# Kernel tuning notes

Measured on AMD Instinct MI355X. Metric: run time of the kernel, lower is better.

## Reference

```python
import jax, jax.numpy as jnp
import numpy as np

D_MODEL = 1024
NUM_HEADS = 16
D_K = D_MODEL // NUM_HEADS
R = 8
ALPHA = 16
SCALING = ALPHA / R


def _lora_linear(x, W, b, A, Bm):
    # base: x @ W.T + b ; lora: (x @ A.T) @ Bm.T * scaling
    base = jnp.einsum('btd,od->bto', x, W) + b
    lora = jnp.einsum('btr,or->bto', jnp.einsum('btd,rd->btr', x, A), Bm) * SCALING
    return base + lora


def setup_inputs() -> dict:
    key = jax.random.key(0)
    ks = jax.random.split(key, 20)
    B, T = 2, 2048
    inp = {
        'q': jax.random.normal(ks[0], (B, T, D_MODEL), jnp.float32),
        'k': jax.random.normal(ks[1], (B, T, D_MODEL), jnp.float32),
        'v': jax.random.normal(ks[2], (B, T, D_MODEL), jnp.float32),
        'mask': jnp.ones((1, 1, T, T), jnp.int32),
    }
    i = 3
    for name in ('q', 'k', 'v'):
        inp[f'W{name}'] = jax.random.normal(ks[i], (D_MODEL, D_MODEL), jnp.float32) * 0.02; i += 1
        inp[f'b{name}'] = jnp.zeros((D_MODEL,), jnp.float32)
        inp[f'A{name}'] = jax.random.normal(ks[i], (R, D_MODEL), jnp.float32) * 0.01; i += 1
        inp[f'B{name}'] = jax.random.normal(ks[i], (D_MODEL, R), jnp.float32) * 0.01; i += 1
    inp['Wo'] = jax.random.normal(ks[i], (D_MODEL, D_MODEL), jnp.float32) * 0.02
    inp['bo'] = jnp.zeros((D_MODEL,), jnp.float32)
    return inp


def reference(q, k, v, mask, Wq, bq, Aq, Bq, Wk, bk, Ak, Bk, Wv, bv, Av, Bv, Wo, bo):
    B, Tq, _ = q.shape
    Tk = k.shape[1]
    Q = _lora_linear(q, Wq, bq, Aq, Bq).reshape(B, Tq, NUM_HEADS, D_K).transpose(0, 2, 1, 3)
    K = _lora_linear(k, Wk, bk, Ak, Bk).reshape(B, Tk, NUM_HEADS, D_K).transpose(0, 2, 1, 3)
    V = _lora_linear(v, Wv, bv, Av, Bv).reshape(B, Tk, NUM_HEADS, D_K).transpose(0, 2, 1, 3)
    scores = jnp.einsum('bhqd,bhkd->bhqk', Q, K) / jnp.sqrt(jnp.float32(D_K))
    scores = jnp.where(mask == 0, jnp.float32(-1e9), scores)
    attn = jax.nn.softmax(scores, axis=-1)
    out = jnp.einsum('bhqk,bhkd->bhqd', attn, V)
    out = out.transpose(0, 2, 1, 3).reshape(B, Tq, D_MODEL)
    return jnp.einsum('btd,od->bto', out, Wo) + bo
```

## Files before the change

### kernel.cpp

```cpp
#include <hip/hip_runtime.h>
#include <stdint.h>

typedef unsigned short u16;
typedef __attribute__((ext_vector_type(4))) float f32x4;
typedef __attribute__((ext_vector_type(4))) uint32_t u32x4;
typedef __attribute__((ext_vector_type(8))) __bf16 bf16x8;

#if __has_builtin(__builtin_amdgcn_exp2f)
#define EXP2(x) __builtin_amdgcn_exp2f(x)
#else
#define EXP2(x) exp2f(x)
#endif

static __device__ __forceinline__ u16 f2bf(float f) {
    union { float f; uint32_t i; } v; v.f = f;
    return (u16)((v.i + 0x7FFFu + ((v.i >> 16) & 1u)) >> 16);
}
static __device__ __forceinline__ uint32_t cvtpk(float lo, float hi) {
    uint32_t r;
    asm("v_cvt_pk_bf16_f32 %0, %1, %2" : "=v"(r) : "v"(lo), "v"(hi));
    return r;
}

static __device__ __forceinline__ void gl2lds16(const u16* g, u16* lds) {
    __builtin_amdgcn_global_load_lds(
        (const __attribute__((address_space(1))) void*)g,
        (__attribute__((address_space(3))) void*)lds, 16, 0, 0);
}

struct PrepArgs {
    const float* csrc[7]; u16* cdst[7];
    const float* A[3]; u16* apk[3];
    const int* mask; int* flags;
};

__global__ __launch_bounds__(256)
void prep_kernel(PrepArgs a) {
    const int bid = blockIdx.x;
    const int tid = threadIdx.x;

    if (bid < 1024) {
        int arr, boff;
        if (bid < 768) { arr = bid >> 8; boff = bid & 255; }
        else { int b2 = bid - 768; arr = 3 + (b2 >> 6); boff = b2 & 63; }
        const float* s = a.csrc[arr] + (size_t)boff * 16384;
        u16* d = a.cdst[arr] + (size_t)boff * 16384;
#pragma unroll
        for (int i = 0; i < 8; ++i) {
            int c = tid + i * 256;
            float4 f0 = *(const float4*)(s + c * 8);
            float4 f1 = *(const float4*)(s + c * 8 + 4);
            u16 o[8];
            o[0] = f2bf(f0.x); o[1] = f2bf(f0.y); o[2] = f2bf(f0.z); o[3] = f2bf(f0.w);
            o[4] = f2bf(f1.x); o[5] = f2bf(f1.y); o[6] = f2bf(f1.z); o[7] = f2bf(f1.w);
            *(uint4*)(d + c * 8) = *(const uint4*)o;
        }
    } else if (bid < 1536) {
        const int b3 = bid - 1024;
        const int qb = b3 & 15, kt = b3 >> 4;
        int ok = 1;
#pragma unroll
        for (int i = 0; i < 8; ++i) {
            int c = tid + i * 256;
            int row = c >> 4, cg = c & 15;
            int4 m4 = *(const int4*)&a.mask[(size_t)(qb * 128 + row) * 2048 + kt * 64 + cg * 4];
            ok &= (m4.x != 0) & (m4.y != 0) & (m4.z != 0) & (m4.w != 0);
        }
        int wall = __all(ok) ? 1 : 0;
        __shared__ int red[4];
        if ((tid & 63) == 0) red[tid >> 6] = wall;
        __syncthreads();
        if (tid == 0) a.flags[qb * 32 + kt] = red[0] & red[1] & red[2] & red[3];
    } else {
        const int z = bid - 1536;
        const float* Az = a.A[z];
        u16* dp = a.apk[z];
#pragma unroll
        for (int i = 0; i < 8; ++i) {
            int pos = tid + i * 256;
            int lane2 = pos & 63;
            int l15_ = lane2 & 15, l4_ = lane2 >> 4;
            int kbkk = pos >> 6;
            int kcol = (kbkk >> 1) * 64 + (kbkk & 1) * 32 + l4_ * 8;
            u16 ob[8] = {0, 0, 0, 0, 0, 0, 0, 0};
            if (l15_ < 8) {
                float4 f0 = *(const float4*)&Az[(size_t)l15_ * 1024 + kcol];
                float4 f1 = *(const float4*)&Az[(size_t)l15_ * 1024 + kcol + 4];
                ob[0] = f2bf(f0.x); ob[1] = f2bf(f0.y); ob[2] = f2bf(f0.z); ob[3] = f2bf(f0.w);
                ob[4] = f2bf(f1.x); ob[5] = f2bf(f1.y); ob[6] = f2bf(f1.z); ob[7] = f2bf(f1.w);
            }
            *(uint4*)&dp[(size_t)pos * 8] = *(const uint4*)ob;
        }
    }
}

struct GemmPtrs { const u16* X; const u16* W; const float* bias; const u16* Ap; const float* Bm; void* out; int transT; float oscale; };
struct GemmArgs { GemmPtrs p[3]; };

#define LST 136
#define LTT 72

template <int WMT, int WNT, int LORA>
__global__ __launch_bounds__(256, 2)
void gemm_kernel(GemmArgs args) {
    constexpr int BM = WMT * 32, BN = WNT * 32;
    constexpr int MBLK = 4096 / BM;
    constexpr int IPA = BM / 32;
    constexpr int IPB = BN / 32;
    __shared__ alignas(16) u16 smem[2][(BM + BN) * 64];

    const GemmPtrs gp = args.p[blockIdx.z];
    const int tid = threadIdx.x;
    const int lane = tid & 63, wave = tid >> 6;
    const int wm = wave >> 1, wn = wave & 1;
    const int l15 = lane & 15, l4 = lane >> 4;
    const int id = blockIdx.x;
    const int m0 = (id % MBLK) * BM, n0 = (id / MBLK) * BN;

    const int srow = lane >> 3;
    const int scol = ((lane & 7) ^ srow) * 8;
    const u16* gA[IPA];
    const u16* gB[IPB];
#pragma unroll
    for (int i = 0; i < IPA; ++i) {
        int q = wave * IPA + i;
        gA[i] = gp.X + (size_t)(m0 + q * 8 + srow) * 1024 + scol;
    }
#pragma unroll
    for (int i = 0; i < IPB; ++i) {
        int q = wave * IPB + i;
        gB[i] = gp.W + (size_t)(n0 + q * 8 + srow) * 1024 + scol;
    }

    const f32x4 fz = {0.f, 0.f, 0.f, 0.f};
    f32x4 acc[WMT][WNT];
#pragma unroll
    for (int i = 0; i < WMT; ++i)
#pragma unroll
        for (int j = 0; j < WNT; ++j) acc[i][j] = fz;
    f32x4 acc_xa[WMT];
    bf16x8 abf[2], abf_n[2];
    if constexpr (LORA) {
#pragma unroll
        for (int i = 0; i < WMT; ++i) acc_xa[i] = fz;
        abf[0] = *(const bf16x8*)&gp.Ap[(size_t)(0 * 64 + lane) * 8];
        abf[1] = *(const bf16x8*)&gp.Ap[(size_t)(1 * 64 + lane) * 8];
    }

#pragma unroll
    for (int i = 0; i < IPA; ++i)
        gl2lds16(gA[i], &smem[0][(wave * IPA + i) * 512]);
#pragma unroll
    for (int i = 0; i < IPB; ++i)
        gl2lds16(gB[i], &smem[0][BM * 64 + (wave * IPB + i) * 512]);
    __syncthreads();

    const int sw = l15 & 7;
    for (int kb = 0; kb < 16; ++kb) {
        const u16* As = &smem[kb & 1][0];
        const u16* Bs = &smem[kb & 1][BM * 64];

        if (kb < 15) {
            if constexpr (LORA) {
                abf_n[0] = *(const bf16x8*)&gp.Ap[(size_t)(((kb + 1) * 2 + 0) * 64 + lane) * 8];
                abf_n[1] = *(const bf16x8*)&gp.Ap[(size_t)(((kb + 1) * 2 + 1) * 64 + lane) * 8];
            }
            u16* An = &smem[(kb + 1) & 1][0];
            u16* Bn = &smem[(kb + 1) & 1][BM * 64];
#pragma unroll
            for (int i = 0; i < IPA; ++i)
                gl2lds16(gA[i] + (kb + 1) * 64, &An[(wave * IPA + i) * 512]);
#pragma unroll
            for (int i = 0; i < IPB; ++i)
                gl2lds16(gB[i] + (kb + 1) * 64, &Bn[(wave * IPB + i) * 512]);
        }

#pragma unroll
        for (int kk2 = 0; kk2 < 2; ++kk2) {
            bf16x8 af[WMT], bfr[WNT];
#pragma unroll
            for (int mt = 0; mt < WMT; ++mt) {
                int x = wm * (WMT * 16) + mt * 16 + l15;
                af[mt] = *(const bf16x8*)&As[x * 64 + (((kk2 * 4 + l4) ^ sw) * 8)];
            }
#pragma unroll
            for (int nt = 0; nt < WNT; ++nt) {
                int y = wn * (WNT * 16) + nt * 16 + l15;
                bfr[nt] = *(const bf16x8*)&Bs[y * 64 + (((kk2 * 4 + l4) ^ sw) * 8)];
            }
#pragma unroll
            for (int mt = 0; mt < WMT; ++mt)
#pragma unroll
                for (int nt = 0; nt < WNT; ++nt)
                    acc[mt][nt] = __builtin_amdgcn_mfma_f32_16x16x32_bf16(af[mt], bfr[nt], acc[mt][nt], 0, 0, 0);
            if constexpr (LORA) {
#pragma unroll
                for (int mt = 0; mt < WMT; ++mt)
                    acc_xa[mt] = __builtin_amdgcn_mfma_f32_16x16x32_bf16(af[mt], abf[kk2], acc_xa[mt], 0, 0, 0);
            }
        }
        if constexpr (LORA) {
            if (kb < 15) { abf[0] = abf_n[0]; abf[1] = abf_n[1]; }
        }

        __syncthreads();
    }

    if constexpr (LORA) {
        float* XAs = (float*)&smem[0][0];
        float* Bms = (float*)&smem[0][BM * 64];
        if (wn == 0 && l15 < 8) {
#pragma unroll
            for (int mt = 0; mt < WMT; ++mt)
#pragma unroll
                for (int r = 0; r < 4; ++r)
                    XAs[(wm * 64 + mt * 16 + l4 * 4 + r) * 8 + l15] = acc_xa[mt][r];
        }
        if (tid < 128) {
            *(float4*)&Bms[tid * 8]     = *(const float4*)&gp.Bm[(size_t)(n0 + tid) * 8];
            *(float4*)&Bms[tid * 8 + 4] = *(const float4*)&gp.Bm[(size_t)(n0 + tid) * 8 + 4];
        }
        __syncthreads();
        const float osc = gp.oscale;
        float bmv[WNT][8], bsv[WNT];
#pragma unroll
        for (int nt = 0; nt < WNT; ++nt) {
            int nloc = wn * 64 + nt * 16 + l15;
            bsv[nt] = gp.bias[n0 + nloc];
#pragma unroll
            for (int q8 = 0; q8 < 8; ++q8) bmv[nt][q8] = Bms[nloc * 8 + q8];
        }
#pragma unroll
        for (int mt = 0; mt < WMT; ++mt)
#pragma unroll
            for (int r = 0; r < 4; ++r) {
                int mloc = wm * 64 + mt * 16 + l4 * 4 + r;
                float xa8[8];
                *(float4*)&xa8[0] = *(const float4*)&XAs[mloc * 8];
                *(float4*)&xa8[4] = *(const float4*)&XAs[mloc * 8 + 4];
#pragma unroll
                for (int nt = 0; nt < WNT; ++nt) {
                    float lora = 0.f;
#pragma unroll
                    for (int q8 = 0; q8 < 8; ++q8) lora += xa8[q8] * bmv[nt][q8];
                    acc[mt][nt][r] = (acc[mt][nt][r] + bsv[nt] + 2.0f * lora) * osc;
                }
            }
        __syncthreads();

        u16* outp = (u16*)gp.out;
        const int bb = m0 >> 11;
        if (gp.transT) {
            u16* Lst = &smem[0][0];
#pragma unroll
            for (int ch = 0; ch < 2; ++ch) {
#pragma unroll
                for (int mt2 = 0; mt2 < 2; ++mt2) {
                    int mt = ch * 2 + mt2;
#pragma unroll
                    for (int nt = 0; nt < WNT; ++nt)
#pragma unroll
                        for (int r = 0; r < 4; ++r)
                            Lst[(wn * 64 + nt * 16 + l15) * LTT + wm * 32 + mt2 * 16 + l4 * 4 + r] =
                                f2bf(acc[mt][nt][r]);
                }
                __syncthreads();
#pragma unroll
                for (int j = 0; j < 4; ++j) {
                    int w = tid + j * 256;
                    int nl = w >> 3, seg = w & 7;
                    uint4 val = *(const uint4*)&Lst[nl * LTT + seg * 8];
                    int n = n0 + nl, hh = n >> 6, dd = n & 63;
                    int c0 = seg * 8;
                    int gm = m0 + (c0 >> 5) * 64 + ch * 32 + (c0 & 31);
                    int t = gm & 2047;
                    *(uint4*)&outp[(((size_t)(bb * 16 + hh)) * 64 + dd) * 2048 + t] = val;
                }
                __syncthreads();
            }
        } else {
            u16* Ls = &smem[0][0];
#pragma unroll
            for (int ch = 0; ch < 2; ++ch) {
#pragma unroll
                for (int mt2 = 0; mt2 < 2; ++mt2) {
                    int mt = ch * 2 + mt2;
#pragma unroll
                    for (int nt = 0; nt < WNT; ++nt)
#pragma unroll
                        for (int r = 0; r < 4; ++r)
                            Ls[(wm * 32 + mt2 * 16 + l4 * 4 + r) * LST + wn * 64 + nt * 16 + l15] =
                                f2bf(acc[mt][nt][r]);
                }
                __syncthreads();
#pragma unroll
                for (int j = 0; j < 4; ++j) {
                    int w = tid + j * 256;
                    int lrow = w >> 4, seg = w & 15;
                    uint4 val = *(const uint4*)&Ls[lrow * LST + seg * 8];
                    int gm = m0 + (lrow >> 5) * 64 + ch * 32 + (lrow & 31);
                    int t = gm & 2047;
                    int n = n0 + seg * 8, hh = n >> 6, dd = n & 63;
                    *(uint4*)&outp[(((size_t)(bb * 16 + hh)) * 2048 + t) * 64 + dd] = val;
                }
                __syncthreads();
            }
        }
    } else {
        float* outp = (float*)gp.out;
#pragma unroll
        for (int mt = 0; mt < WMT; ++mt)
#pragma unroll
            for (int r = 0; r < 4; ++r) {
                int m = m0 + wm * (WMT * 16) + mt * 16 + l4 * 4 + r;
#pragma unroll
                for (int nt = 0; nt < WNT; ++nt) {
                    int n = n0 + wn * (WNT * 16) + nt * 16 + l15;
                    outp[(size_t)m * 1024 + n] = acc[mt][nt][r] + gp.bias[n];
                }
            }
    }
}


__global__ __launch_bounds__(256, 4)
void attn_kernel(const u16* __restrict__ QKV, const int* __restrict__ mask,
                 const int* __restrict__ flags, u16* __restrict__ Xo) {
    const int qb = blockIdx.x >> 5;
    const int bh = blockIdx.x & 31;
    const int b = bh >> 4, h = bh & 15;
    const int tid = threadIdx.x;
    const int lane = tid & 63, wave = tid >> 6;
    const int l15 = lane & 15, l4 = lane >> 4;

    __shared__ alignas(16) u16 Ks[2][64 * 64];
    __shared__ alignas(16) u16 Vts[2][64 * 64];

    const size_t plane = (size_t)2 * 16 * 2048 * 64;
    const u16* Qg = QKV + (size_t)(b * 16 + h) * 2048 * 64;
    const u16* Kg = Qg + plane;
    const u16* Vg = Kg + plane;

    const int srow = lane >> 3;
    const int scol = ((lane & 7) ^ srow) * 8;

    const u16* kbase[2];
    const u16* vbase[2];
#pragma unroll
    for (int i = 0; i < 2; ++i) {
        int qq = wave * 2 + i;
        int kc = 16 * (qq & 1) + 8 * (srow >> 2) + 4 * ((qq >> 1) & 1) + (srow & 3) + 32 * (qq >> 2);
        kbase[i] = Kg + (size_t)kc * 64 + scol;
        vbase[i] = Vg + (size_t)(qq * 8 + srow) * 2048 + scol;
    }

    bf16x8 qa[2];
#pragma unroll
    for (int kk2 = 0; kk2 < 2; ++kk2)
        qa[kk2] = *(const bf16x8*)&Qg[(size_t)(qb * 64 + wave * 16 + l15) * 64 + kk2 * 32 + l4 * 8];

    const f32x4 fz = {0.f, 0.f, 0.f, 0.f};
    f32x4 accO[4];
#pragma unroll
    for (int dt = 0; dt < 4; ++dt) accO[dt] = fz;
    f32x4 accSum = fz;
    const u32x4 onesw = {0x3F803F80u, 0x3F803F80u, 0x3F803F80u, 0x3F803F80u};
    const bf16x8 onesf = __builtin_bit_cast(bf16x8, onesw);

#pragma unroll
    for (int i = 0; i < 2; ++i) {
        int qq = wave * 2 + i;
        gl2lds16(kbase[i], &Ks[0][qq * 512]);
        gl2lds16(vbase[i], &Vts[0][qq * 512]);
    }
    __syncthreads();

    for (int kt = 0; kt < 32; ++kt) {
        const u16* Kc = &Ks[kt & 1][0];
        const u16* Vc = &Vts[kt & 1][0];

        if (kt < 31) {
            u16* Kn = &Ks[(kt + 1) & 1][0];
            u16* Vn = &Vts[(kt + 1) & 1][0];
#pragma unroll
            for (int i = 0; i < 2; ++i) {
                int qq = wave * 2 + i;
                gl2lds16(kbase[i] + (size_t)(kt + 1) * 4096, &Kn[qq * 512]);
                gl2lds16(vbase[i] + (size_t)(kt + 1) * 64, &Vn[qq * 512]);
            }
        }

        f32x4 accS[4];
#pragma unroll
        for (int j = 0; j < 4; ++j) accS[j] = fz;
#pragma unroll
        for (int kk2 = 0; kk2 < 2; ++kk2) {
            bf16x8 kf[4];
#pragma unroll
            for (int j = 0; j < 4; ++j)
                kf[j] = *(const bf16x8*)&Kc[(j * 16 + l15) * 64 + (((kk2 * 4 + l4) ^ (l15 & 7)) * 8)];
            __builtin_amdgcn_s_setprio(1);
#pragma unroll
            for (int j = 0; j < 4; ++j)
                accS[j] = __builtin_amdgcn_mfma_f32_16x16x32_bf16(kf[j], qa[kk2], accS[j], 0, 0, 0);
            __builtin_amdgcn_s_setprio(0);
        }

        if (flags[(qb >> 1) * 32 + kt] == 0) {
            int qrow = qb * 64 + wave * 16 + l15;
#pragma unroll
            for (int j = 0; j < 4; ++j)
#pragma unroll
                for (int r = 0; r < 4; ++r) {
                    int kcol = kt * 64 + 8 * l4 + 4 * (j & 1) + r + 32 * (j >> 1);
                    if (mask[(size_t)qrow * 2048 + kcol] == 0) accS[j][r] = -1e9f;
                }
        }

#pragma unroll
        for (int j = 0; j < 4; ++j)
#pragma unroll
            for (int r = 0; r < 4; ++r)
                accS[j][r] = EXP2(accS[j][r]);

        u32x4 paw0, paw1;
        paw0[0] = cvtpk(accS[0][0], accS[0][1]); paw0[1] = cvtpk(accS[0][2], accS[0][3]);
        paw0[2] = cvtpk(accS[1][0], accS[1][1]); paw0[3] = cvtpk(accS[1][2], accS[1][3]);
        paw1[0] = cvtpk(accS[2][0], accS[2][1]); paw1[1] = cvtpk(accS[2][2], accS[2][3]);
        paw1[2] = cvtpk(accS[3][0], accS[3][1]); paw1[3] = cvtpk(accS[3][2], accS[3][3]);
        bf16x8 pa[2];
        pa[0] = __builtin_bit_cast(bf16x8, paw0);
        pa[1] = __builtin_bit_cast(bf16x8, paw1);

#pragma unroll
        for (int kk2 = 0; kk2 < 2; ++kk2) {
            bf16x8 vf[4];
#pragma unroll
            for (int dt = 0; dt < 4; ++dt)
                vf[dt] = *(const bf16x8*)&Vc[(dt * 16 + l15) * 64 + (((kk2 * 4 + l4) ^ (l15 & 7)) * 8)];
            __builtin_amdgcn_s_setprio(1);
#pragma unroll
            for (int dt = 0; dt < 4; ++dt)
                accO[dt] = __builtin_amdgcn_mfma_f32_16x16x32_bf16(pa[kk2], vf[dt], accO[dt], 0, 0, 0);
            accSum = __builtin_amdgcn_mfma_f32_16x16x32_bf16(pa[kk2], onesf, accSum, 0, 0, 0);
            __builtin_amdgcn_s_setprio(0);
        }

        __syncthreads();
    }

    float inv[4];
#pragma unroll
    for (int r = 0; r < 4; ++r) inv[r] = 1.0f / accSum[r];

    u16* Es = &Ks[0][0];
#pragma unroll
    for (int dt = 0; dt < 4; ++dt)
#pragma unroll
        for (int r = 0; r < 4; ++r) {
            int prow = wave * 16 + l4 * 4 + r;
            Es[prow * 64 + (((dt * 2 + (l15 >> 3)) ^ (prow & 7)) * 8) + (l15 & 7)] =
                f2bf(accO[dt][r] * inv[r]);
        }
    __syncthreads();
#pragma unroll
    for (int j = 0; j < 2; ++j) {
        int w = tid + j * 256;
        int row = w >> 3, seg = w & 7;
        uint4 val = *(const uint4*)&Es[row * 64 + ((seg ^ (row & 7)) * 8)];
        int t = qb * 64 + row;
        *(uint4*)&Xo[((size_t)(b * 2048 + t)) * 1024 + h * 64 + seg * 8] = val;
    }
}

extern "C" void kernel_launch(void* const* d_in, const int* in_sizes, int n_in,
                              void* d_out, int out_size, void* d_ws, size_t ws_size,
                              hipStream_t stream) {
    const float* q    = (const float*)d_in[0];
    const float* k    = (const float*)d_in[1];
    const float* v    = (const float*)d_in[2];
    const int*   mask = (const int*)d_in[3];
    const float* Wq = (const float*)d_in[4];
    const float* bq = (const float*)d_in[5];
    const float* Aq = (const float*)d_in[6];
    const float* Bq = (const float*)d_in[7];
    const float* Wk = (const float*)d_in[8];
    const float* bk = (const float*)d_in[9];
    const float* Ak = (const float*)d_in[10];
    const float* Bk = (const float*)d_in[11];
    const float* Wv = (const float*)d_in[12];
    const float* bv = (const float*)d_in[13];
    const float* Av = (const float*)d_in[14];
    const float* Bv = (const float*)d_in[15];
    const float* Wo = (const float*)d_in[16];
    const float* bo = (const float*)d_in[17];

    char* ws = (char*)d_ws;
    u16*   QKV   = (u16*)ws;
    u16*   qb16  = (u16*)(ws + 25165824);
    u16*   kb16  = (u16*)(ws + 33554432);
    u16*   vb16  = (u16*)(ws + 41943040);
    u16*   Wqb   = (u16*)(ws + 50331648);
    u16*   Wkb   = (u16*)(ws + 52428800);
    u16*   Wvb   = (u16*)(ws + 54525952);
    u16*   Wob   = (u16*)(ws + 56623104);
    u16*   Apk   = (u16*)(ws + 58720256);
    int*   flags = (int*)(ws + 59113472);
    u16*   Xbuf  = qb16;

    PrepArgs pa;
    pa.csrc[0] = q;  pa.csrc[1] = k;  pa.csrc[2] = v;
    pa.csrc[3] = Wq; pa.csrc[4] = Wk; pa.csrc[5] = Wv; pa.csrc[6] = Wo;
    pa.cdst[0] = qb16; pa.cdst[1] = kb16; pa.cdst[2] = vb16;
    pa.cdst[3] = Wqb;  pa.cdst[4] = Wkb;  pa.cdst[5] = Wvb; pa.cdst[6] = Wob;
    pa.A[0] = Aq; pa.A[1] = Ak; pa.A[2] = Av;
    pa.apk[0] = Apk; pa.apk[1] = Apk + 16384; pa.apk[2] = Apk + 32768;
    pa.mask = mask; pa.flags = flags;
    prep_kernel<<<dim3(1539), dim3(256), 0, stream>>>(pa);

    const float QSCALE = 0.1803368801f;
    GemmArgs g1;
    g1.p[0] = GemmPtrs{qb16, Wqb, bq, Apk,         Bq, (void*)QKV,             0, QSCALE};
    g1.p[1] = GemmPtrs{kb16, Wkb, bk, Apk + 16384, Bk, (void*)(QKV + 4194304), 0, 1.0f};
    g1.p[2] = GemmPtrs{vb16, Wvb, bv, Apk + 32768, Bv, (void*)(QKV + 8388608), 1, 1.0f};
    gemm_kernel<4, 4, 1><<<dim3(256, 1, 3), dim3(256), 0, stream>>>(g1);

    attn_kernel<<<dim3(1024), dim3(256), 0, stream>>>(QKV, mask, flags, Xbuf);

    GemmArgs g2;
    g2.p[0] = GemmPtrs{Xbuf, Wob, bo, nullptr, nullptr, d_out, 0, 1.0f};
    g2.p[1] = g2.p[0];
    g2.p[2] = g2.p[0];
    gemm_kernel<2, 4, 0><<<dim3(512, 1, 1), dim3(256), 0, stream>>>(g2);
}
```

Before: 247.3 us.

## Store K and V in MFMA fragment order and load directly from global

The QKV projection epilogue now writes K and V in a per-lane MFMA fragment layout. This lets the attention kernel load its K/V operands straight from global memory as contiguous 16-byte vectors. It drops the LDS double buffering, the global-to-LDS copies and the per-tile barriers. The cost is that every wave (and every query block) now fetches K/V through the caches on its own instead of sharing them via LDS, and load latency is no longer hidden by an explicit prefetch.

```diff
diff --git a/kernel.cpp b/kernel.cpp
--- a/kernel.cpp
+++ b/kernel.cpp
@@ -94,7 +94,7 @@
     }
 }
 
-struct GemmPtrs { const u16* X; const u16* W; const float* bias; const u16* Ap; const float* Bm; void* out; int transT; float oscale; };
+struct GemmPtrs { const u16* X; const u16* W; const float* bias; const u16* Ap; const float* Bm; void* out; int transT; int kfrag; float oscale; };
 struct GemmArgs { GemmPtrs p[3]; };
 
 #define LST 136
@@ -274,12 +274,18 @@
                     int c0 = seg * 8;
                     int gm = m0 + (c0 >> 5) * 64 + ch * 32 + (c0 & 31);
                     int t = gm & 2047;
-                    *(uint4*)&outp[(((size_t)(bb * 16 + hh)) * 64 + dd) * 2048 + t] = val;
+                    int kt = t >> 6, k_in = t & 63;
+                    int kk2v = k_in >> 5, l4v = (k_in >> 3) & 3;
+                    int dtv = dd >> 4, l15v = dd & 15;
+                    size_t addr = ((size_t)(bb * 16 + hh)) * 131072 +
+                                  (size_t)(((kt * 2 + kk2v) * 4 + dtv) * 64 + l4v * 16 + l15v) * 8;
+                    *(uint4*)&outp[addr] = val;
                 }
                 __syncthreads();
             }
         } else {
             u16* Ls = &smem[0][0];
+            const int kfr = gp.kfrag;
 #pragma unroll
             for (int ch = 0; ch < 2; ++ch) {
 #pragma unroll
@@ -301,7 +307,17 @@
                     int gm = m0 + (lrow >> 5) * 64 + ch * 32 + (lrow & 31);
                     int t = gm & 2047;
                     int n = n0 + seg * 8, hh = n >> 6, dd = n & 63;
-                    *(uint4*)&outp[(((size_t)(bb * 16 + hh)) * 2048 + t) * 64 + dd] = val;
+                    if (kfr) {
+                        int kt = t >> 6, m63 = t & 63;
+                        int jj = 2 * (m63 >> 5) + ((m63 >> 2) & 1);
+                        int l15f = 4 * ((m63 >> 3) & 3) + (m63 & 3);
+                        int kk2f = dd >> 5, l4f = (dd >> 3) & 3;
+                        size_t addr = ((size_t)(bb * 16 + hh)) * 131072 +
+                                      (size_t)(((kt * 2 + kk2f) * 4 + jj) * 64 + l4f * 16 + l15f) * 8;
+                        *(uint4*)&outp[addr] = val;
+                    } else {
+                        *(uint4*)&outp[(((size_t)(bb * 16 + hh)) * 2048 + t) * 64 + dd] = val;
+                    }
                 }
                 __syncthreads();
             }
@@ -333,26 +349,11 @@
     const int lane = tid & 63, wave = tid >> 6;
     const int l15 = lane & 15, l4 = lane >> 4;
 
-    __shared__ alignas(16) u16 Ks[2][64 * 64];
-    __shared__ alignas(16) u16 Vts[2][64 * 64];
-
-    const size_t plane = (size_t)2 * 16 * 2048 * 64;
-    const u16* Qg = QKV + (size_t)(b * 16 + h) * 2048 * 64;
-    const u16* Kg = Qg + plane;
-    const u16* Vg = Kg + plane;
-
-    const int srow = lane >> 3;
-    const int scol = ((lane & 7) ^ srow) * 8;
-
-    const u16* kbase[2];
-    const u16* vbase[2];
-#pragma unroll
-    for (int i = 0; i < 2; ++i) {
-        int qq = wave * 2 + i;
-        int kc = 16 * (qq & 1) + 8 * (srow >> 2) + 4 * ((qq >> 1) & 1) + (srow & 3) + 32 * (qq >> 2);
-        kbase[i] = Kg + (size_t)kc * 64 + scol;
-        vbase[i] = Vg + (size_t)(qq * 8 + srow) * 2048 + scol;
-    }
+    __shared__ alignas(16) u16 Es[64 * 64];
+
+    const u16* Qg = QKV + (size_t)(b * 16 + h) * 131072;
+    const u16* Kf = QKV + 4194304 + (size_t)(b * 16 + h) * 131072;
+    const u16* Vf = QKV + 8388608 + (size_t)(b * 16 + h) * 131072;
 
     bf16x8 qa[2];
 #pragma unroll
@@ -367,42 +368,22 @@
     const u32x4 onesw = {0x3F803F80u, 0x3F803F80u, 0x3F803F80u, 0x3F803F80u};
     const bf16x8 onesf = __builtin_bit_cast(bf16x8, onesw);
 
-#pragma unroll
-    for (int i = 0; i < 2; ++i) {
-        int qq = wave * 2 + i;
-        gl2lds16(kbase[i], &Ks[0][qq * 512]);
-        gl2lds16(vbase[i], &Vts[0][qq * 512]);
-    }
-    __syncthreads();
-
     for (int kt = 0; kt < 32; ++kt) {
-        const u16* Kc = &Ks[kt & 1][0];
-        const u16* Vc = &Vts[kt & 1][0];
-
-        if (kt < 31) {
-            u16* Kn = &Ks[(kt + 1) & 1][0];
-            u16* Vn = &Vts[(kt + 1) & 1][0];
-#pragma unroll
-            for (int i = 0; i < 2; ++i) {
-                int qq = wave * 2 + i;
-                gl2lds16(kbase[i] + (size_t)(kt + 1) * 4096, &Kn[qq * 512]);
-                gl2lds16(vbase[i] + (size_t)(kt + 1) * 64, &Vn[qq * 512]);
-            }
-        }
-
         f32x4 accS[4];
 #pragma unroll
         for (int j = 0; j < 4; ++j) accS[j] = fz;
+        bf16x8 kf[2][4];
+#pragma unroll
+        for (int kk2 = 0; kk2 < 2; ++kk2)
+#pragma unroll
+            for (int j = 0; j < 4; ++j)
+                kf[kk2][j] = *(const bf16x8*)&Kf[(size_t)(((kt * 2 + kk2) * 4 + j) * 64 + lane) * 8];
 #pragma unroll
         for (int kk2 = 0; kk2 < 2; ++kk2) {
-            bf16x8 kf[4];
+            __builtin_amdgcn_s_setprio(1);
 #pragma unroll
             for (int j = 0; j < 4; ++j)
-                kf[j] = *(const bf16x8*)&Kc[(j * 16 + l15) * 64 + (((kk2 * 4 + l4) ^ (l15 & 7)) * 8)];
-            __builtin_amdgcn_s_setprio(1);
-#pragma unroll
-            for (int j = 0; j < 4; ++j)
-                accS[j] = __builtin_amdgcn_mfma_f32_16x16x32_bf16(kf[j], qa[kk2], accS[j], 0, 0, 0);
+                accS[j] = __builtin_amdgcn_mfma_f32_16x16x32_bf16(kf[kk2][j], qa[kk2], accS[j], 0, 0, 0);
             __builtin_amdgcn_s_setprio(0);
         }
 
@@ -437,7 +418,7 @@
             bf16x8 vf[4];
 #pragma unroll
             for (int dt = 0; dt < 4; ++dt)
-                vf[dt] = *(const bf16x8*)&Vc[(dt * 16 + l15) * 64 + (((kk2 * 4 + l4) ^ (l15 & 7)) * 8)];
+                vf[dt] = *(const bf16x8*)&Vf[(size_t)(((kt * 2 + kk2) * 4 + dt) * 64 + lane) * 8];
             __builtin_amdgcn_s_setprio(1);
 #pragma unroll
             for (int dt = 0; dt < 4; ++dt)
@@ -445,15 +426,12 @@
             accSum = __builtin_amdgcn_mfma_f32_16x16x32_bf16(pa[kk2], onesf, accSum, 0, 0, 0);
             __builtin_amdgcn_s_setprio(0);
         }
-
-        __syncthreads();
     }
 
     float inv[4];
 #pragma unroll
     for (int r = 0; r < 4; ++r) inv[r] = 1.0f / accSum[r];
 
-    u16* Es = &Ks[0][0];
 #pragma unroll
     for (int dt = 0; dt < 4; ++dt)
 #pragma unroll
@@ -520,15 +498,15 @@
 
     const float QSCALE = 0.1803368801f;
     GemmArgs g1;
-    g1.p[0] = GemmPtrs{qb16, Wqb, bq, Apk,         Bq, (void*)QKV,             0, QSCALE};
-    g1.p[1] = GemmPtrs{kb16, Wkb, bk, Apk + 16384, Bk, (void*)(QKV + 4194304), 0, 1.0f};
-    g1.p[2] = GemmPtrs{vb16, Wvb, bv, Apk + 32768, Bv, (void*)(QKV + 8388608), 1, 1.0f};
+    g1.p[0] = GemmPtrs{qb16, Wqb, bq, Apk,         Bq, (void*)QKV,             0, 0, QSCALE};
+    g1.p[1] = GemmPtrs{kb16, Wkb, bk, Apk + 16384, Bk, (void*)(QKV + 4194304), 0, 1, 1.0f};
+    g1.p[2] = GemmPtrs{vb16, Wvb, bv, Apk + 32768, Bv, (void*)(QKV + 8388608), 1, 0, 1.0f};
     gemm_kernel<4, 4, 1><<<dim3(256, 1, 3), dim3(256), 0, stream>>>(g1);
 
     attn_kernel<<<dim3(1024), dim3(256), 0, stream>>>(QKV, mask, flags, Xbuf);
 
     GemmArgs g2;
-    g2.p[0] = GemmPtrs{Xbuf, Wob, bo, nullptr, nullptr, d_out, 0, 1.0f};
+    g2.p[0] = GemmPtrs{Xbuf, Wob, bo, nullptr, nullptr, d_out, 0, 0, 1.0f};
     g2.p[1] = g2.p[0];
     g2.p[2] = g2.p[0];
     gemm_kernel<2, 4, 0><<<dim3(512, 1, 1), dim3(256), 0, stream>>>(g2);
```

After: 264.2 us. 1.07x slower.
